# Performance work log

Hardware: AMD Instinct MI355X
Metric: run time of the kernel (lower is better)

The kernel has to match this reference:

```python
import jax, jax.numpy as jnp
import numpy as np

B, VH, VL, EP = 4, 130, 120, 256
DIN, DEP, D, H, NL = 256, 128, 512, 16, 8
HID = 4 * D

def _pe(x, base=1000.0):
    # sinusoidal positional encoding (base=1000 as in the module)
    L, Dm = x.shape[-2], x.shape[-1]
    pos = jnp.arange(L, dtype=jnp.float32)
    ch = jnp.arange(Dm, dtype=jnp.float32)
    ang = pos[:, None] / (base ** (2.0 * ch / ch[-1]))[None]
    enc = jnp.where(ch % 2 == 0, jnp.sin(ang), jnp.cos(ang))
    return x + enc

def _ln(x, g, b):
    m = x.mean(-1, keepdims=True)
    v = ((x - m) ** 2).mean(-1, keepdims=True)
    return (x - m) / jnp.sqrt(v + 1e-5) * g + b

def _gmha(x, rots, trans, mask_bias, qkv_w, out_w, out_b, g, b, r_s, d_s):
    # ESM3 geometric multi-head attention (algorithm 6)
    xn = _ln(x, g, b)
    qkv = (xn @ qkv_w.T).reshape(x.shape[0], x.shape[1], 5, H, 3)  # [B,L,5,H,3]
    qkv = jnp.einsum('brid,brfhd->brfhi', rots, qkv)               # rotate into global frame
    Qr, Kr, Qd, Kd, V = (qkv[..., f, :, :] for f in range(5))
    scale = 3.0 ** -0.5
    Ar = jnp.einsum('bihd,bjhd->bijh', Qr, Kr) * jax.nn.softplus(r_s) * scale
    qd = Qd + trans[:, :, None, :]
    kd = Kd + trans[:, :, None, :]
    dist = jnp.linalg.norm(qd[:, :, None] - kd[:, None], axis=-1)  # [B,i,j,H]
    logits = Ar - dist * jax.nn.softplus(d_s) * scale + mask_bias[..., None]
    A = jax.nn.softmax(logits, axis=2)
    o = jnp.einsum('bijh,bjhd->bihd', A, V)
    o = jnp.einsum('brji,brhj->brhi', rots, o)                     # rotate back (R^T)
    return o.reshape(x.shape[0], x.shape[1], H * 3) @ out_w.T + out_b

def _swiglu(x, g, b, w12, w3):
    # SwiGLU transition (dropout is identity in eval)
    h = _ln(x, g, b) @ w12.T
    a, v = jnp.split(h, 2, axis=-1)
    return (jax.nn.silu(a) * v) @ w3.T

def _forward(vh_x, vl_x, vh_rots, vh_trans, vl_rots, vl_trans, ep_feats, ep_rots, ep_trans,
             vh_emb_w, vl_emb_w, tgt_emb_w, qkv_w, out_w, out_b, ln_g, ln_b, r_scale, d_scale,
             ln2_g, ln2_b, w12, w3, out_vh_w, out_vh_gate_w, out_vh_gate_b,
             out_vl_w, out_vl_gate_w, out_vl_gate_b, vh_mask, vl_mask, ep_mask):
    emb = jnp.concatenate([_pe(vh_x @ vh_emb_w.T), _pe(vl_x @ vl_emb_w.T), ep_feats @ tgt_emb_w.T], axis=1)
    rots = jnp.concatenate([vh_rots, vl_rots, ep_rots], axis=1)
    trans = jnp.concatenate([vh_trans, vl_trans, ep_trans], axis=1)
    mask = jnp.concatenate([vh_mask, vl_mask, ep_mask], axis=1)
    mask_bias = jnp.where(mask[:, :, None] | mask[:, None, :], -1e9, 0.0)
    for i in range(NL):
        emb = emb + _gmha(emb, rots, trans, mask_bias, qkv_w[i], out_w[i], out_b[i],
                          ln_g[i], ln_b[i], r_scale[i], d_scale[i])
        emb = emb + _swiglu(emb, ln2_g[i], ln2_b[i], w12[i], w3[i])
    vh_e, vl_e = emb[:, :VH], emb[:, VH:VH + VL]
    vh_upd = (vh_e @ out_vh_w.T) * jax.nn.sigmoid(vh_e @ out_vh_gate_w.T + out_vh_gate_b)
    vl_upd = (vl_e @ out_vl_w.T) * jax.nn.sigmoid(vl_e @ out_vl_gate_w.T + out_vl_gate_b)
    vh_out = jnp.where(~vh_mask[..., None], vh_x + vh_upd, vh_x)
    vl_out = jnp.where(~vl_mask[..., None], vl_x + vl_upd, vl_x)
    return vh_out, vl_out

def setup_inputs():
    key = jax.random.key(0)
    ks = iter(jax.random.split(key, 40))
    s = 0.02
    return dict(
        vh_x=jax.random.normal(next(ks), (B, VH, DIN)),
        vl_x=jax.random.normal(next(ks), (B, VL, DIN)),
        vh_rots=jax.random.normal(next(ks), (B, VH, 3, 3)),
        vh_trans=jax.random.normal(next(ks), (B, VH, 3)),
        vl_rots=jax.random.normal(next(ks), (B, VL, 3, 3)),
        vl_trans=jax.random.normal(next(ks), (B, VL, 3)),
        ep_feats=jax.random.normal(next(ks), (B, EP, DEP)),
        ep_rots=jax.random.normal(next(ks), (B, EP, 3, 3)),
        ep_trans=jax.random.normal(next(ks), (B, EP, 3)),
        vh_mask=jnp.zeros((B, VH), dtype=bool),
        vl_mask=jnp.zeros((B, VL), dtype=bool),
        ep_mask=jax.random.randint(next(ks), (B, EP), 0, 2).astype(bool),
        vh_emb_w=jax.random.normal(next(ks), (D, DIN)) * s,
        vl_emb_w=jax.random.normal(next(ks), (D, DIN)) * s,
        tgt_emb_w=jax.random.normal(next(ks), (D, DEP)) * s,
        qkv_w=jax.random.normal(next(ks), (NL, H * 15, D)) * s,
        out_w=jax.random.normal(next(ks), (NL, D, H * 3)) * s,
        out_b=jnp.zeros((NL, D)),
        ln_g=jnp.ones((NL, D)), ln_b=jnp.zeros((NL, D)),
        r_scale=jnp.zeros((NL, H)), d_scale=jnp.zeros((NL, H)),
        ln2_g=jnp.ones((NL, D)), ln2_b=jnp.zeros((NL, D)),
        w12=jax.random.normal(next(ks), (NL, 2 * HID, D)) * s,
        w3=jax.random.normal(next(ks), (NL, D, HID)) * s,
        out_vh_w=jax.random.normal(next(ks), (DIN, D)) * s,
        out_vh_gate_w=jax.random.normal(next(ks), (DIN, D)) * s,
        out_vh_gate_b=jnp.full((DIN,), -2.0),
        out_vl_w=jax.random.normal(next(ks), (DIN, D)) * s,
        out_vl_gate_w=jax.random.normal(next(ks), (DIN, D)) * s,
        out_vl_gate_b=jnp.full((DIN,), -2.0),
    )

def reference(vh_x, vl_x, vh_rots, vh_trans, vl_rots, vl_trans, ep_feats, ep_rots, ep_trans,
              vh_mask, vl_mask, ep_mask,
              vh_emb_w, vl_emb_w, tgt_emb_w, qkv_w, out_w, out_b, ln_g, ln_b, r_scale, d_scale,
              ln2_g, ln2_b, w12, w3, out_vh_w, out_vh_gate_w, out_vh_gate_b,
              out_vl_w, out_vl_gate_w, out_vl_gate_b):
    return _forward(vh_x, vl_x, vh_rots, vh_trans, vl_rots, vl_trans, ep_feats, ep_rots, ep_trans,
                    vh_emb_w, vl_emb_w, tgt_emb_w, qkv_w, out_w, out_b, ln_g, ln_b, r_scale, d_scale,
                    ln2_g, ln2_b, w12, w3, out_vh_w, out_vh_gate_w, out_vh_gate_b,
                    out_vl_w, out_vl_gate_w, out_vl_gate_b, vh_mask, vl_mask, ep_mask)
```

## Files before the change

kernel.cpp:

```cpp
#include <hip/hip_runtime.h>
#include <hip/hip_bf16.h>
#include <math.h>
#include <stdint.h>

#define B_ 4
#define VH_ 130
#define VL_ 120
#define EP_ 256
#define R_ 506
#define RP_ 512
#define DIN_ 256
#define DEP_ 128
#define D_ 512
#define H_ 16
#define NL_ 8
#define HID_ 2048

#define MODE_STORE 0
#define MODE_ADD_BIAS 1

typedef _Float16 half8 __attribute__((ext_vector_type(8)));
typedef float f32x4 __attribute__((ext_vector_type(4)));

#define ASYNC16(ldsdst, gsrc)                                                  \
  __builtin_amdgcn_global_load_lds(                                            \
      (const __attribute__((address_space(1))) unsigned int*)(gsrc),           \
      (__attribute__((address_space(3))) unsigned int*)(ldsdst), 16, 0, 0)

__global__ __launch_bounds__(256) void gemm16sw_kernel(
    const _Float16* __restrict__ A, const _Float16* __restrict__ Wa,
    const _Float16* __restrict__ Wv, _Float16* __restrict__ Gh,
    int M, int K) {
  __shared__ _Float16 Al[4][4096];
  __shared__ _Float16 Ba[4][2048];
  __shared__ _Float16 Bv[4][2048];

  const int t = threadIdx.x;
  const int nbm = (M + 127) >> 7;
  const int nwg = gridDim.x;
  int bid = blockIdx.x;
  if ((nwg & 7) == 0) {
    int q = nwg >> 3;
    bid = (bid & 7) * q + (bid >> 3);
  }
  const int bm = bid % nbm, bn = bid / nbm;
  const int lane = t & 63;
  const int w = t >> 6;
  const int wm = w >> 1, wn = w & 1;

  const int r0 = t >> 2;
  const int cp = t & 3;
  const int gc = cp ^ ((r0 >> 1) & 3);
  int gr0 = bm * 128 + r0;       if (gr0 >= M) gr0 = M - 1;
  int gr1 = bm * 128 + 64 + r0;  if (gr1 >= M) gr1 = M - 1;
  const int gcol = bn * 64 + r0;
  const _Float16* pA0 = A + (size_t)gr0 * K + gc * 8;
  const _Float16* pA1 = A + (size_t)gr1 * K + gc * 8;
  const _Float16* pBa = Wa + (size_t)gcol * K + gc * 8;
  const _Float16* pBv = Wv + (size_t)gcol * K + gc * 8;

#define STAGE(buf, kt)                                                         \
  do {                                                                         \
    ASYNC16(&Al[buf][t * 8], pA0 + (size_t)(kt) * 32);                         \
    ASYNC16(&Al[buf][2048 + t * 8], pA1 + (size_t)(kt) * 32);                  \
    ASYNC16(&Ba[buf][t * 8], pBa + (size_t)(kt) * 32);                         \
    ASYNC16(&Bv[buf][t * 8], pBv + (size_t)(kt) * 32);                         \
  } while (0)

  f32x4 aca[4][2], acv[4][2];
#pragma unroll
  for (int i = 0; i < 4; i++)
#pragma unroll
    for (int j = 0; j < 2; j++) {
      aca[i][j] = (f32x4){0.f, 0.f, 0.f, 0.f};
      acv[i][j] = (f32x4){0.f, 0.f, 0.f, 0.f};
    }

  const int nt = K >> 5;
  STAGE(0, 0); STAGE(1, 1); STAGE(2, 2);

  const int rl = lane & 15;
  const int ca = (lane >> 4) ^ ((rl >> 1) & 3);
  for (int kt = 0; kt < nt; ++kt) {
    if (kt < nt - 2)       asm volatile("s_waitcnt vmcnt(8)" ::: "memory");
    else if (kt == nt - 2) asm volatile("s_waitcnt vmcnt(4)" ::: "memory");
    else                   asm volatile("s_waitcnt vmcnt(0)" ::: "memory");
    __builtin_amdgcn_s_barrier();
    const int buf = kt & 3;
    const _Float16* Ab  = &Al[buf][(wm * 64 + rl) * 32 + ca * 8];
    const _Float16* Bab = &Ba[buf][(wn * 32 + rl) * 32 + ca * 8];
    const _Float16* Bvb = &Bv[buf][(wn * 32 + rl) * 32 + ca * 8];
    half8 af[4], bfa[2], bfv[2];
#pragma unroll
    for (int i = 0; i < 4; i++) af[i] = *(const half8*)(Ab + i * 512);
#pragma unroll
    for (int j = 0; j < 2; j++) {
      bfa[j] = *(const half8*)(Bab + j * 512);
      bfv[j] = *(const half8*)(Bvb + j * 512);
    }
#pragma unroll
    for (int i = 0; i < 4; i++)
#pragma unroll
      for (int j = 0; j < 2; j++) {
        aca[i][j] = __builtin_amdgcn_mfma_f32_16x16x32_f16(af[i], bfa[j],
                                                           aca[i][j], 0, 0, 0);
        acv[i][j] = __builtin_amdgcn_mfma_f32_16x16x32_f16(af[i], bfv[j],
                                                           acv[i][j], 0, 0, 0);
      }
    if (kt + 3 < nt) STAGE((kt + 3) & 3, kt + 3);
  }
#undef STAGE

  const int rb = bm * 128 + wm * 64 + ((lane >> 4) << 2);
  const int cb = bn * 64 + wn * 32 + (lane & 15);
#pragma unroll
  for (int i = 0; i < 4; i++) {
#pragma unroll
    for (int j = 0; j < 2; j++) {
      int col = cb + j * 16;
#pragma unroll
      for (int q = 0; q < 4; q++) {
        int row = rb + i * 16 + q;
        if (row >= M) continue;
        float a = aca[i][j][q];
        float v = acv[i][j][q];
        Gh[(size_t)row * HID_ + col] = (_Float16)((a / (1.f + expf(-a))) * v);
      }
    }
  }
}

__global__ __launch_bounds__(256) void gemm16b_kernel(
    const _Float16* __restrict__ A, const _Float16* __restrict__ W,
    float* __restrict__ C, const float* __restrict__ bias,
    int M, int N, int K, int mode, int crpb, int cR, int cbase, int pe) {
  __shared__ _Float16 Al[4][2048];
  __shared__ _Float16 Bl[4][2048];

  const int t = threadIdx.x;
  const int nbm = (M + 63) >> 6;
  const int nwg = gridDim.x;
  int bid = blockIdx.x;
  if ((nwg & 7) == 0) {
    int q = nwg >> 3;
    bid = (bid & 7) * q + (bid >> 3);
  }
  const int bm = bid % nbm, bn = bid / nbm;
  const int lane = t & 63;
  const int w = t >> 6;
  const int wm = w >> 1, wn = w & 1;

  const int r0 = t >> 2;
  const int cp = t & 3;
  const int gc = cp ^ ((r0 >> 1) & 3);
  int gr = bm * 64 + r0;    if (gr >= M) gr = M - 1;
  int gcol = bn * 64 + r0;  if (gcol >= N) gcol = N - 1;
  const _Float16* pA = A + (size_t)gr * K + gc * 8;
  const _Float16* pB = W + (size_t)gcol * K + gc * 8;

#define STAGE(buf, kt)                                                         \
  do {                                                                         \
    ASYNC16(&Al[buf][t * 8], pA + (size_t)(kt) * 32);                          \
    ASYNC16(&Bl[buf][t * 8], pB + (size_t)(kt) * 32);                          \
  } while (0)

  f32x4 acc[2][2];
#pragma unroll
  for (int i = 0; i < 2; i++)
#pragma unroll
    for (int j = 0; j < 2; j++) acc[i][j] = (f32x4){0.f, 0.f, 0.f, 0.f};

  const int nt = K >> 5;
  STAGE(0, 0); STAGE(1, 1); STAGE(2, 2);

  const int rl = lane & 15;
  const int ca = (lane >> 4) ^ ((rl >> 1) & 3);
  for (int kt = 0; kt < nt; ++kt) {
    if (kt < nt - 2)       asm volatile("s_waitcnt vmcnt(4)" ::: "memory");
    else if (kt == nt - 2) asm volatile("s_waitcnt vmcnt(2)" ::: "memory");
    else                   asm volatile("s_waitcnt vmcnt(0)" ::: "memory");
    __builtin_amdgcn_s_barrier();
    const int buf = kt & 3;
    half8 af[2], bf[2];
#pragma unroll
    for (int i = 0; i < 2; i++)
      af[i] = *(const half8*)&Al[buf][(wm * 32 + i * 16 + rl) * 32 + ca * 8];
#pragma unroll
    for (int j = 0; j < 2; j++)
      bf[j] = *(const half8*)&Bl[buf][(wn * 32 + j * 16 + rl) * 32 + ca * 8];
#pragma unroll
    for (int i = 0; i < 2; i++)
#pragma unroll
      for (int j = 0; j < 2; j++)
        acc[i][j] = __builtin_amdgcn_mfma_f32_16x16x32_f16(af[i], bf[j],
                                                           acc[i][j], 0, 0, 0);
    if (kt + 3 < nt) STAGE((kt + 3) & 3, kt + 3);
  }
#undef STAGE

  const float PEK = -0.02703623196464017f;
  const int rb = bm * 64 + wm * 32 + ((lane >> 4) << 2);
  const int cb = bn * 64 + wn * 32 + (lane & 15);
#pragma unroll
  for (int i = 0; i < 2; i++) {
#pragma unroll
    for (int j = 0; j < 2; j++) {
      int col = cb + j * 16;
      if (col >= N) continue;
#pragma unroll
      for (int q = 0; q < 4; q++) {
        int row = rb + i * 16 + q;
        if (row >= M) continue;
        int crow = (row / crpb) * cR + cbase + row % crpb;
        size_t idx = (size_t)crow * N + col;
        float v = acc[i][j][q];
        if (pe) {
          float pos = (float)(row % crpb);
          float ang = pos * expf((float)col * PEK);
          v += (col & 1) ? cosf(ang) : sinf(ang);
        }
        if (mode == MODE_STORE) C[idx] = v;
        else {
          float bb = bias ? bias[col] : 0.f;
          C[idx] = C[idx] + v + bb;
        }
      }
    }
  }
}

__global__ __launch_bounds__(256) void gemm16gate_kernel(
    const _Float16* __restrict__ A, const _Float16* __restrict__ Wv,
    const _Float16* __restrict__ Wg, const float* __restrict__ x,
    const float* __restrict__ gb, const int* __restrict__ mask,
    float* __restrict__ out, int M, int K, int arpb, int aR, int abase) {
  __shared__ _Float16 Al[4][2048];
  __shared__ _Float16 Bva[4][2048];
  __shared__ _Float16 Bga[4][2048];

  const int t = threadIdx.x;
  const int nbm = (M + 63) >> 6;
  const int nwg = gridDim.x;
  int bid = blockIdx.x;
  if ((nwg & 7) == 0) {
    int q = nwg >> 3;
    bid = (bid & 7) * q + (bid >> 3);
  }
  const int bm = bid % nbm, bn = bid / nbm;
  const int lane = t & 63;
  const int w = t >> 6;
  const int wm = w >> 1, wn = w & 1;

  const int r0 = t >> 2;
  const int cp = t & 3;
  const int gc = cp ^ ((r0 >> 1) & 3);
  int gr = bm * 64 + r0;  if (gr >= M) gr = M - 1;
  int ar = (gr / arpb) * aR + abase + gr % arpb;
  const int gcol = bn * 64 + r0;
  const _Float16* pA  = A + (size_t)ar * K + gc * 8;
  const _Float16* pBv = Wv + (size_t)gcol * K + gc * 8;
  const _Float16* pBg = Wg + (size_t)gcol * K + gc * 8;

#define STAGE(buf, kt)                                                         \
  do {                                                                         \
    ASYNC16(&Al[buf][t * 8], pA + (size_t)(kt) * 32);                          \
    ASYNC16(&Bva[buf][t * 8], pBv + (size_t)(kt) * 32);                        \
    ASYNC16(&Bga[buf][t * 8], pBg + (size_t)(kt) * 32);                        \
  } while (0)

  f32x4 acv[2][2], acg[2][2];
#pragma unroll
  for (int i = 0; i < 2; i++)
#pragma unroll
    for (int j = 0; j < 2; j++) {
      acv[i][j] = (f32x4){0.f, 0.f, 0.f, 0.f};
      acg[i][j] = (f32x4){0.f, 0.f, 0.f, 0.f};
    }

  const int nt = K >> 5;
  STAGE(0, 0); STAGE(1, 1); STAGE(2, 2);

  const int rl = lane & 15;
  const int ca = (lane >> 4) ^ ((rl >> 1) & 3);
  for (int kt = 0; kt < nt; ++kt) {
    if (kt < nt - 2)       asm volatile("s_waitcnt vmcnt(6)" ::: "memory");
    else if (kt == nt - 2) asm volatile("s_waitcnt vmcnt(3)" ::: "memory");
    else                   asm volatile("s_waitcnt vmcnt(0)" ::: "memory");
    __builtin_amdgcn_s_barrier();
    const int buf = kt & 3;
    half8 af[2], bv[2], bg2[2];
#pragma unroll
    for (int i = 0; i < 2; i++)
      af[i] = *(const half8*)&Al[buf][(wm * 32 + i * 16 + rl) * 32 + ca * 8];
#pragma unroll
    for (int j = 0; j < 2; j++) {
      bv[j] = *(const half8*)&Bva[buf][(wn * 32 + j * 16 + rl) * 32 + ca * 8];
      bg2[j] = *(const half8*)&Bga[buf][(wn * 32 + j * 16 + rl) * 32 + ca * 8];
    }
#pragma unroll
    for (int i = 0; i < 2; i++)
#pragma unroll
      for (int j = 0; j < 2; j++) {
        acv[i][j] = __builtin_amdgcn_mfma_f32_16x16x32_f16(af[i], bv[j],
                                                           acv[i][j], 0, 0, 0);
        acg[i][j] = __builtin_amdgcn_mfma_f32_16x16x32_f16(af[i], bg2[j],
                                                           acg[i][j], 0, 0, 0);
      }
    if (kt + 3 < nt) STAGE((kt + 3) & 3, kt + 3);
  }
#undef STAGE

  const int rb = bm * 64 + wm * 32 + ((lane >> 4) << 2);
  const int cb = bn * 64 + wn * 32 + (lane & 15);
#pragma unroll
  for (int i = 0; i < 2; i++) {
#pragma unroll
    for (int j = 0; j < 2; j++) {
      int col = cb + j * 16;
#pragma unroll
      for (int q = 0; q < 4; q++) {
        int row = rb + i * 16 + q;
        if (row >= M) continue;
        size_t idx = (size_t)row * DIN_ + col;
        float xv = x[idx];
        float res;
        if (mask[row]) {
          res = xv;
        } else {
          float gate = 1.f / (1.f + expf(-(acg[i][j][q] + gb[col])));
          res = xv + acv[i][j][q] * gate;
        }
        out[idx] = res;
      }
    }
  }
}

__global__ __launch_bounds__(256) void ln_kernel(
    const float* __restrict__ x, const float* __restrict__ g,
    const float* __restrict__ b, _Float16* __restrict__ out) {
  const int row = blockIdx.x;
  const int t = threadIdx.x;
  const float* xr = x + (size_t)row * D_;
  float v0 = xr[t], v1 = xr[t + 256];
  float s = v0 + v1, s2 = v0 * v0 + v1 * v1;
#pragma unroll
  for (int o = 32; o > 0; o >>= 1) {
    s += __shfl_down(s, o);
    s2 += __shfl_down(s2, o);
  }
  __shared__ float w1[4], w2[4], mv[2];
  const int w = t >> 6;
  if ((t & 63) == 0) { w1[w] = s; w2[w] = s2; }
  __syncthreads();
  if (t == 0) {
    float ss = w1[0] + w1[1] + w1[2] + w1[3];
    float ss2 = w2[0] + w2[1] + w2[2] + w2[3];
    float mean = ss * (1.f / D_);
    float var = ss2 * (1.f / D_) - mean * mean;
    mv[0] = mean;
    mv[1] = rsqrtf(var + 1e-5f);
  }
  __syncthreads();
  float mean = mv[0], inv = mv[1];
  _Float16* orow = out + (size_t)row * D_;
  orow[t] = (_Float16)((v0 - mean) * inv * g[t] + b[t]);
  orow[t + 256] = (_Float16)((v1 - mean) * inv * g[t + 256] + b[t + 256]);
}

struct ThSegs {
  const float* src[13];
  _Float16* dst[13];
  int cum[14];
};
__global__ void tohalf_multi_kernel(ThSegs sg) {
  int total = sg.cum[13];
  for (int i = blockIdx.x * blockDim.x + threadIdx.x; i < total;
       i += gridDim.x * blockDim.x) {
    int s = 0;
    while (i >= sg.cum[s + 1]) s++;
    int off = i - sg.cum[s];
    const float4* p = (const float4*)(sg.src[s] + (size_t)off * 8);
    float4 x = p[0], y = p[1];
    half8 h = {(_Float16)x.x, (_Float16)x.y, (_Float16)x.z, (_Float16)x.w,
               (_Float16)y.x, (_Float16)y.y, (_Float16)y.z, (_Float16)y.w};
    *(half8*)(sg.dst[s] + (size_t)off * 8) = h;
  }
}

__global__ void tohalf_kernel(const float* __restrict__ src,
                              _Float16* __restrict__ dst, int n8) {
  for (int i = blockIdx.x * blockDim.x + threadIdx.x; i < n8;
       i += gridDim.x * blockDim.x) {
    const float4* s = (const float4*)(src + (size_t)i * 8);
    float4 x = s[0], y = s[1];
    half8 h = {(_Float16)x.x, (_Float16)x.y, (_Float16)x.z, (_Float16)x.w,
               (_Float16)y.x, (_Float16)y.y, (_Float16)y.z, (_Float16)y.w};
    *(half8*)(dst + (size_t)i * 8) = h;
  }
}

__global__ void transpose_ow_kernel(const float* __restrict__ out_w,
                                    float* __restrict__ owT) {
  int idx = blockIdx.x * blockDim.x + threadIdx.x;
  const int total = NL_ * 48 * D_;
  if (idx >= total) return;
  int l = idx / (48 * D_);
  int rem = idx % (48 * D_);
  int k = rem / D_;
  int c = rem % D_;
  owT[idx] = out_w[(size_t)l * D_ * 48 + (size_t)c * 48 + k];
}

__global__ void prep_kernel(
    const float* __restrict__ vh_rots, const float* __restrict__ vh_trans,
    const float* __restrict__ vl_rots, const float* __restrict__ vl_trans,
    const float* __restrict__ ep_rots, const float* __restrict__ ep_trans,
    const int* __restrict__ vh_mask, const int* __restrict__ vl_mask,
    const int* __restrict__ ep_mask, float* __restrict__ rots,
    float* __restrict__ trans, int* __restrict__ mask,
    int* __restrict__ maskp, float* __restrict__ Kt, float* __restrict__ PKt,
    float* __restrict__ Vt) {
  int idx = blockIdx.x * blockDim.x + threadIdx.x;
  if (idx < B_ * RP_) {
    int b = idx >> 9, r = idx & (RP_ - 1);
    if (r >= R_) {
      maskp[idx] = 1;
      return;
    }
    const float* sr; const float* st; int sm;
    if (r < VH_) {
      sr = vh_rots + (size_t)(b * VH_ + r) * 9;
      st = vh_trans + (size_t)(b * VH_ + r) * 3;
      sm = vh_mask[b * VH_ + r];
    } else if (r < VH_ + VL_) {
      int rr = r - VH_;
      sr = vl_rots + (size_t)(b * VL_ + rr) * 9;
      st = vl_trans + (size_t)(b * VL_ + rr) * 3;
      sm = vl_mask[b * VL_ + rr];
    } else {
      int rr = r - VH_ - VL_;
      sr = ep_rots + (size_t)(b * EP_ + rr) * 9;
      st = ep_trans + (size_t)(b * EP_ + rr) * 3;
      sm = ep_mask[b * EP_ + rr];
    }
    int lin = b * R_ + r;
    maskp[idx] = sm;
    mask[lin] = sm;
#pragma unroll
    for (int k = 0; k < 9; k++) rots[(size_t)lin * 9 + k] = sr[k];
#pragma unroll
    for (int k = 0; k < 3; k++) trans[(size_t)lin * 3 + k] = st[k];
  } else {
    int p = idx - B_ * RP_;
    const int per = B_ * H_ * 3 * (RP_ - R_);
    if (p >= 3 * per) return;
    int a = p / per;
    int q = p % per;
    int chan = q / (RP_ - R_), jj = q % (RP_ - R_);
    float* dst = (a == 0) ? Kt : (a == 1) ? PKt : Vt;
    dst[(size_t)chan * RP_ + R_ + jj] = 0.f;
  }
}

__global__ __launch_bounds__(128) void rotate_kernel(
    const float* __restrict__ qkv_raw, const float* __restrict__ rots,
    const float* __restrict__ trans, float* __restrict__ Qrow,
    float* __restrict__ PQrow, float* __restrict__ Kt,
    float* __restrict__ PKt, float* __restrict__ Vt) {
  const int blk = blockIdx.x;
  const int b = blk / R_;
  const int r = blk % R_;
  const int t = threadIdx.x;
  __shared__ float Rm[9], tr[3], raw[240];
  if (t < 9) Rm[t] = rots[(size_t)blk * 9 + t];
  if (t >= 9 && t < 12) tr[t - 9] = trans[(size_t)blk * 3 + (t - 9)];
  for (int i = t; i < 240; i += 128) raw[i] = qkv_raw[(size_t)blk * 240 + i];
  __syncthreads();
  if (t < 80) {
    int f = t / 16, h = t % 16;
    float x = raw[f * 48 + h * 3 + 0];
    float y = raw[f * 48 + h * 3 + 1];
    float z = raw[f * 48 + h * 3 + 2];
    float r0 = Rm[0] * x + Rm[1] * y + Rm[2] * z;
    float r1 = Rm[3] * x + Rm[4] * y + Rm[5] * z;
    float r2 = Rm[6] * x + Rm[7] * y + Rm[8] * z;
    if (f == 2 || f == 3) { r0 += tr[0]; r1 += tr[1]; r2 += tr[2]; }
    if (f == 0 || f == 2) {
      float* dst = (f == 0) ? Qrow : PQrow;
      size_t o = (size_t)blk * 48 + h * 3;
      dst[o] = r0; dst[o + 1] = r1; dst[o + 2] = r2;
    } else {
      float* dst = (f == 1) ? Kt : (f == 3) ? PKt : Vt;
      size_t base = ((size_t)(b * H_ + h) * 3) * RP_ + r;
      dst[base] = r0; dst[base + RP_] = r1; dst[base + 2 * RP_] = r2;
    }
  }
}

__global__ __launch_bounds__(256) void attn2_kernel(
    const float* __restrict__ Qrow, const float* __restrict__ PQrow,
    const float* __restrict__ Kt, const float* __restrict__ PKt,
    const float* __restrict__ Vt, const float* __restrict__ rots,
    const int* __restrict__ mask, const int* __restrict__ maskp,
    const float* __restrict__ rs, const float* __restrict__ ds,
    const float* __restrict__ owT, const float* __restrict__ out_b,
    float* __restrict__ emb) {
  const int blk = blockIdx.x;
  const int b = blk / (R_ / 2);
  const int ip = blk % (R_ / 2);
  const int i0 = ip * 2;
  const int t = threadIdx.x;
  const int lane = t & 63;
  const int w = t >> 6;

  __shared__ float qs[2][48], ps[2][48], og[2][48];
  __shared__ float crs[16], cds[16];
  __shared__ int mi[2];

  if (t < 96) {
    int io = t / 48, k2 = t % 48;
    int i = i0 + io;
    qs[io][k2] = Qrow[((size_t)(b * R_ + i)) * 48 + k2];
    ps[io][k2] = PQrow[((size_t)(b * R_ + i)) * 48 + k2];
  } else if (t < 112) {
    int h = t - 96;
    const float sc = 0.57735026918962576f;
    crs[h] = log1pf(expf(rs[h])) * sc;
    cds[h] = log1pf(expf(ds[h])) * sc;
  } else if (t < 114) {
    mi[t - 112] = mask[b * R_ + i0 + (t - 112)];
  }
  __syncthreads();

  float mb[8];
#pragma unroll
  for (int jb = 0; jb < 8; jb++) {
    int j = jb * 64 + lane;
    mb[jb] = maskp[b * RP_ + j] ? -1e9f : 0.f;
  }
  const float bi0 = mi[0] ? -1e9f : 0.f;
  const float bi1 = mi[1] ? -1e9f : 0.f;

  for (int hh = 0; hh < 4; hh++) {
    const int h = hh * 4 + w;
    const float sA = crs[h], sD = cds[h];
    const float qx0 = qs[0][h * 3], qy0 = qs[0][h * 3 + 1], qz0 = qs[0][h * 3 + 2];
    const float px0 = ps[0][h * 3], py0 = ps[0][h * 3 + 1], pz0 = ps[0][h * 3 + 2];
    const float qx1 = qs[1][h * 3], qy1 = qs[1][h * 3 + 1], qz1 = qs[1][h * 3 + 2];
    const float px1 = ps[1][h * 3], py1 = ps[1][h * 3 + 1], pz1 = ps[1][h * 3 + 2];
    const float* kb = Kt + ((size_t)(b * H_ + h) * 3) * RP_;
    const float* pb = PKt + ((size_t)(b * H_ + h) * 3) * RP_;
    const float* vb = Vt + ((size_t)(b * H_ + h) * 3) * RP_;

    float l0[8], l1[8];
    float m0 = -3e38f, m1 = -3e38f;
#pragma unroll
    for (int jb = 0; jb < 8; jb++) {
      int j = jb * 64 + lane;
      float kx = kb[j], ky = kb[j + RP_], kz = kb[j + 2 * RP_];
      float pkx = pb[j], pky = pb[j + RP_], pkz = pb[j + 2 * RP_];
      float dx0 = px0 - pkx, dy0 = py0 - pky, dz0 = pz0 - pkz;
      float d0 = sqrtf(dx0 * dx0 + dy0 * dy0 + dz0 * dz0);
      l0[jb] = (qx0 * kx + qy0 * ky + qz0 * kz) * sA - d0 * sD + mb[jb] + bi0;
      m0 = fmaxf(m0, l0[jb]);
      float dx1 = px1 - pkx, dy1 = py1 - pky, dz1 = pz1 - pkz;
      float d1 = sqrtf(dx1 * dx1 + dy1 * dy1 + dz1 * dz1);
      l1[jb] = (qx1 * kx + qy1 * ky + qz1 * kz) * sA - d1 * sD + mb[jb] + bi1;
      m1 = fmaxf(m1, l1[jb]);
    }
#pragma unroll
    for (int s = 1; s < 64; s <<= 1) {
      m0 = fmaxf(m0, __shfl_xor(m0, s));
      m1 = fmaxf(m1, __shfl_xor(m1, s));
    }
    float s0 = 0.f, s1 = 0.f;
    float ox0 = 0.f, oy0 = 0.f, oz0 = 0.f, ox1 = 0.f, oy1 = 0.f, oz1 = 0.f;
#pragma unroll
    for (int jb = 0; jb < 8; jb++) {
      int j = jb * 64 + lane;
      float p0 = expf(l0[jb] - m0);
      float p1 = expf(l1[jb] - m1);
      s0 += p0; s1 += p1;
      float vx = vb[j], vy = vb[j + RP_], vz = vb[j + 2 * RP_];
      ox0 += p0 * vx; oy0 += p0 * vy; oz0 += p0 * vz;
      ox1 += p1 * vx; oy1 += p1 * vy; oz1 += p1 * vz;
    }
#pragma unroll
    for (int s = 1; s < 64; s <<= 1) {
      s0 += __shfl_xor(s0, s); s1 += __shfl_xor(s1, s);
      ox0 += __shfl_xor(ox0, s); oy0 += __shfl_xor(oy0, s); oz0 += __shfl_xor(oz0, s);
      ox1 += __shfl_xor(ox1, s); oy1 += __shfl_xor(oy1, s); oz1 += __shfl_xor(oz1, s);
    }
    if (lane == 0) {
      og[0][h * 3] = ox0 / s0; og[0][h * 3 + 1] = oy0 / s0; og[0][h * 3 + 2] = oz0 / s0;
      og[1][h * 3] = ox1 / s1; og[1][h * 3 + 1] = oy1 / s1; og[1][h * 3 + 2] = oz1 / s1;
    }
  }
  __syncthreads();
  float r0v0 = 0.f, r0v1 = 0.f;
  if (t < 48) {
    int h = t / 3, i3 = t % 3;
    const float* Rm0 = rots + ((size_t)(b * R_ + i0)) * 9;
    const float* Rm1 = rots + ((size_t)(b * R_ + i0 + 1)) * 9;
    r0v0 = Rm0[0 + i3] * og[0][h * 3 + 0] + Rm0[3 + i3] * og[0][h * 3 + 1] +
           Rm0[6 + i3] * og[0][h * 3 + 2];
    r0v1 = Rm1[0 + i3] * og[1][h * 3 + 0] + Rm1[3 + i3] * og[1][h * 3 + 1] +
           Rm1[6 + i3] * og[1][h * 3 + 2];
  }
  __syncthreads();
  if (t < 48) { og[0][t] = r0v0; og[1][t] = r0v1; }
  __syncthreads();
#pragma unroll
  for (int io = 0; io < 2; io++) {
    float* erow = emb + ((size_t)(b * R_ + i0 + io)) * D_;
#pragma unroll
    for (int half = 0; half < 2; half++) {
      int c = half * 256 + t;
      float a0 = 0.f, a1 = 0.f, a2 = 0.f, a3 = 0.f;
#pragma unroll
      for (int k = 0; k < 48; k += 4) {
        a0 += og[io][k + 0] * owT[(size_t)(k + 0) * D_ + c];
        a1 += og[io][k + 1] * owT[(size_t)(k + 1) * D_ + c];
        a2 += og[io][k + 2] * owT[(size_t)(k + 2) * D_ + c];
        a3 += og[io][k + 3] * owT[(size_t)(k + 3) * D_ + c];
      }
      erow[c] += out_b[c] + ((a0 + a1) + (a2 + a3));
    }
  }
}

extern "C" void kernel_launch(void* const* d_in, const int* in_sizes, int n_in,
                              void* d_out, int out_size, void* d_ws, size_t ws_size,
                              hipStream_t stream) {
  const float* vh_x = (const float*)d_in[0];
  const float* vl_x = (const float*)d_in[1];
  const float* vh_rots = (const float*)d_in[2];
  const float* vh_trans = (const float*)d_in[3];
  const float* vl_rots = (const float*)d_in[4];
  const float* vl_trans = (const float*)d_in[5];
  const float* ep_feats = (const float*)d_in[6];
  const float* ep_rots = (const float*)d_in[7];
  const float* ep_trans = (const float*)d_in[8];
  const int* vh_mask = (const int*)d_in[9];
  const int* vl_mask = (const int*)d_in[10];
  const int* ep_mask = (const int*)d_in[11];
  const float* vh_emb_w = (const float*)d_in[12];
  const float* vl_emb_w = (const float*)d_in[13];
  const float* tgt_emb_w = (const float*)d_in[14];
  const float* qkv_w = (const float*)d_in[15];
  const float* out_w = (const float*)d_in[16];
  const float* out_b = (const float*)d_in[17];
  const float* ln_g = (const float*)d_in[18];
  const float* ln_b = (const float*)d_in[19];
  const float* r_scale = (const float*)d_in[20];
  const float* d_scale = (const float*)d_in[21];
  const float* ln2_g = (const float*)d_in[22];
  const float* ln2_b = (const float*)d_in[23];
  const float* w12 = (const float*)d_in[24];
  const float* w3 = (const float*)d_in[25];
  const float* out_vh_w = (const float*)d_in[26];
  const float* out_vh_gate_w = (const float*)d_in[27];
  const float* out_vh_gate_b = (const float*)d_in[28];
  const float* out_vl_w = (const float*)d_in[29];
  const float* out_vl_gate_w = (const float*)d_in[30];
  const float* out_vl_gate_b = (const float*)d_in[31];

  const int BR = B_ * R_;

  uint8_t* P = (uint8_t*)d_ws;
  auto alloc = [&](size_t bytes) {
    uint8_t* p = P;
    P += (bytes + 255) & ~(size_t)255;
    return p;
  };
  float* emb = (float*)alloc((size_t)BR * D_ * 4);
  _Float16* xnh = (_Float16*)alloc((size_t)BR * D_ * 2);
  float* qkvr = (float*)alloc((size_t)BR * 240 * 4);
  float* Qrow = (float*)alloc((size_t)BR * 48 * 4);
  float* PQrow = (float*)alloc((size_t)BR * 48 * 4);
  float* Kt = (float*)alloc((size_t)B_ * H_ * 3 * RP_ * 4);
  float* PKt = (float*)alloc((size_t)B_ * H_ * 3 * RP_ * 4);
  float* Vt = (float*)alloc((size_t)B_ * H_ * 3 * RP_ * 4);
  _Float16* ghalf = (_Float16*)alloc((size_t)BR * HID_ * 2);
  float* rots_c = (float*)alloc((size_t)BR * 9 * 4);
  float* trans_c = (float*)alloc((size_t)BR * 3 * 4);
  int* mask_c = (int*)alloc((size_t)BR * 4);
  int* maskp = (int*)alloc((size_t)B_ * RP_ * 4);
  float* owT = (float*)alloc((size_t)NL_ * 48 * D_ * 4);
  _Float16* embh = (_Float16*)alloc((size_t)BR * D_ * 2);
  _Float16* qkvh = (_Float16*)alloc((size_t)NL_ * 240 * D_ * 2);
  _Float16* w12h = (_Float16*)alloc((size_t)NL_ * 2 * HID_ * D_ * 2);
  _Float16* w3h = (_Float16*)alloc((size_t)NL_ * D_ * HID_ * 2);
  _Float16* vhxh = (_Float16*)alloc((size_t)B_ * VH_ * DIN_ * 2);
  _Float16* vlxh = (_Float16*)alloc((size_t)B_ * VL_ * DIN_ * 2);
  _Float16* eph = (_Float16*)alloc((size_t)B_ * EP_ * DEP_ * 2);
  _Float16* vhewh = (_Float16*)alloc((size_t)D_ * DIN_ * 2);
  _Float16* vlewh = (_Float16*)alloc((size_t)D_ * DIN_ * 2);
  _Float16* tgewh = (_Float16*)alloc((size_t)D_ * DEP_ * 2);
  _Float16* ovhw = (_Float16*)alloc((size_t)DIN_ * D_ * 2);
  _Float16* ovhgw = (_Float16*)alloc((size_t)DIN_ * D_ * 2);
  _Float16* ovlw = (_Float16*)alloc((size_t)DIN_ * D_ * 2);
  _Float16* ovlgw = (_Float16*)alloc((size_t)DIN_ * D_ * 2);

  {
    ThSegs sg;
    const float* srcs[13] = {qkv_w, w12, w3, vh_x, vl_x, ep_feats,
                             vh_emb_w, vl_emb_w, tgt_emb_w,
                             out_vh_w, out_vh_gate_w, out_vl_w, out_vl_gate_w};
    _Float16* dsts[13] = {qkvh, w12h, w3h, vhxh, vlxh, eph,
                          vhewh, vlewh, tgewh, ovhw, ovhgw, ovlw, ovlgw};
    int n8s[13] = {NL_ * 240 * D_ / 8, NL_ * 2 * HID_ * D_ / 8,
                   NL_ * D_ * HID_ / 8, B_ * VH_ * DIN_ / 8,
                   B_ * VL_ * DIN_ / 8, B_ * EP_ * DEP_ / 8,
                   D_ * DIN_ / 8, D_ * DIN_ / 8, D_ * DEP_ / 8,
                   DIN_ * D_ / 8, DIN_ * D_ / 8, DIN_ * D_ / 8, DIN_ * D_ / 8};
    int c = 0;
    for (int i = 0; i < 13; i++) {
      sg.src[i] = srcs[i]; sg.dst[i] = dsts[i];
      sg.cum[i] = c; c += n8s[i];
    }
    sg.cum[13] = c;
    tohalf_multi_kernel<<<2048, 256, 0, stream>>>(sg);
  }

  {
    int total = NL_ * 48 * D_;
    transpose_ow_kernel<<<(total + 255) / 256, 256, 0, stream>>>(out_w, owT);
  }

  {
    int total = B_ * RP_ + 3 * B_ * H_ * 3 * (RP_ - R_);
    prep_kernel<<<(total + 255) / 256, 256, 0, stream>>>(
        vh_rots, vh_trans, vl_rots, vl_trans, ep_rots, ep_trans, vh_mask,
        vl_mask, ep_mask, rots_c, trans_c, mask_c, maskp, Kt, PKt, Vt);
  }

  auto gemm16b = [&](const _Float16* A, const _Float16* W, float* C,
                     const float* bias, int M, int N, int K, int mode,
                     int crpb, int cR, int cbase, int pe) {
    int nbm = (M + 63) / 64, nbn = (N + 63) / 64;
    gemm16b_kernel<<<nbm * nbn, 256, 0, stream>>>(A, W, C, bias, M, N, K, mode,
                                                  crpb, cR, cbase, pe);
  };

  gemm16b(vhxh, vhewh, emb, nullptr, B_ * VH_, D_, DIN_, MODE_STORE,
          VH_, R_, 0, 1);
  gemm16b(vlxh, vlewh, emb, nullptr, B_ * VL_, D_, DIN_, MODE_STORE,
          VL_, R_, VH_, 1);
  gemm16b(eph, tgewh, emb, nullptr, B_ * EP_, D_, DEP_, MODE_STORE,
          EP_, R_, VH_ + VL_, 0);

  for (int l = 0; l < NL_; l++) {
    const _Float16* qwh = qkvh + (size_t)l * 240 * D_;
    const float* owTl = owT + (size_t)l * 48 * D_;
    const float* obias = out_b + (size_t)l * D_;
    const float* lg = ln_g + (size_t)l * D_;
    const float* lb = ln_b + (size_t)l * D_;
    const float* l2g = ln2_g + (size_t)l * D_;
    const float* l2b = ln2_b + (size_t)l * D_;
    const float* rs = r_scale + (size_t)l * H_;
    const float* dsc = d_scale + (size_t)l * H_;
    const _Float16* w12ah = w12h + (size_t)l * 2 * HID_ * D_;
    const _Float16* w12bh = w12ah + (size_t)HID_ * D_;
    const _Float16* w3lh = w3h + (size_t)l * D_ * HID_;

    ln_kernel<<<BR, 256, 0, stream>>>(emb, lg, lb, xnh);
    gemm16b(xnh, qwh, qkvr, nullptr, BR, 240, D_, MODE_STORE, BR, BR, 0, 0);
    rotate_kernel<<<BR, 128, 0, stream>>>(qkvr, rots_c, trans_c, Qrow, PQrow,
                                          Kt, PKt, Vt);
    attn2_kernel<<<B_ * (R_ / 2), 256, 0, stream>>>(
        Qrow, PQrow, Kt, PKt, Vt, rots_c, mask_c, maskp, rs, dsc, owTl, obias,
        emb);

    ln_kernel<<<BR, 256, 0, stream>>>(emb, l2g, l2b, xnh);
    {
      int nbm = (BR + 127) / 128, nbn = HID_ / 64;
      gemm16sw_kernel<<<nbm * nbn, 256, 0, stream>>>(xnh, w12ah, w12bh, ghalf,
                                                     BR, D_);
    }
    gemm16b(ghalf, w3lh, emb, nullptr, BR, D_, HID_, MODE_ADD_BIAS,
            BR, BR, 0, 0);
  }

  tohalf_kernel<<<1024, 256, 0, stream>>>(emb, embh, BR * D_ / 8);
  {
    int M = B_ * VH_;
    int nbm = (M + 63) / 64;
    gemm16gate_kernel<<<nbm * 4, 256, 0, stream>>>(
        embh, ovhw, ovhgw, vh_x, out_vh_gate_b, vh_mask, (float*)d_out, M, D_,
        VH_, R_, 0);
  }
  {
    int M = B_ * VL_;
    int nbm = (M + 63) / 64;
    gemm16gate_kernel<<<nbm * 4, 256, 0, stream>>>(
        embh, ovlw, ovlgw, vl_x, out_vl_gate_b, vl_mask,
        (float*)d_out + (size_t)B_ * VH_ * DIN_, M, D_, VL_, R_, VH_);
  }
}
```

Before: 1.108 ms.

## Use one wave per head in attention and convert sixteen floats per thread

The attention kernel now launches 1024 threads per block, so each of the 16 heads gets its own wavefront instead of four waves looping over four heads each. The output projection is spread across all 1024 threads, one output element per thread. Separately, the fp32-to-fp16 conversion kernel now handles 16 elements per thread instead of 8, which halves the per-element segment-search overhead. The larger blocks raise per-block parallelism but cap register use under a 1024-thread launch bound and may reduce how many blocks fit per CU.

```diff
diff --git a/kernel.cpp b/kernel.cpp
--- a/kernel.cpp
+++ b/kernel.cpp
@@ -380,11 +380,15 @@
     int s = 0;
     while (i >= sg.cum[s + 1]) s++;
     int off = i - sg.cum[s];
-    const float4* p = (const float4*)(sg.src[s] + (size_t)off * 8);
-    float4 x = p[0], y = p[1];
-    half8 h = {(_Float16)x.x, (_Float16)x.y, (_Float16)x.z, (_Float16)x.w,
-               (_Float16)y.x, (_Float16)y.y, (_Float16)y.z, (_Float16)y.w};
-    *(half8*)(sg.dst[s] + (size_t)off * 8) = h;
+    const float4* p = (const float4*)(sg.src[s] + (size_t)off * 16);
+    float4 x = p[0], y = p[1], z = p[2], w = p[3];
+    half8 h0 = {(_Float16)x.x, (_Float16)x.y, (_Float16)x.z, (_Float16)x.w,
+                (_Float16)y.x, (_Float16)y.y, (_Float16)y.z, (_Float16)y.w};
+    half8 h1 = {(_Float16)z.x, (_Float16)z.y, (_Float16)z.z, (_Float16)z.w,
+                (_Float16)w.x, (_Float16)w.y, (_Float16)w.z, (_Float16)w.w};
+    half8* d = (half8*)(sg.dst[s] + (size_t)off * 16);
+    d[0] = h0;
+    d[1] = h1;
   }
 }
 
@@ -498,7 +502,7 @@
   }
 }
 
-__global__ __launch_bounds__(256) void attn2_kernel(
+__global__ __launch_bounds__(1024) void attn2_kernel(
     const float* __restrict__ Qrow, const float* __restrict__ PQrow,
     const float* __restrict__ Kt, const float* __restrict__ PKt,
     const float* __restrict__ Vt, const float* __restrict__ rots,
@@ -512,7 +516,7 @@
   const int i0 = ip * 2;
   const int t = threadIdx.x;
   const int lane = t & 63;
-  const int w = t >> 6;
+  const int h = t >> 6;
 
   __shared__ float qs[2][48], ps[2][48], og[2][48];
   __shared__ float crs[16], cds[16];
@@ -524,10 +528,10 @@
     qs[io][k2] = Qrow[((size_t)(b * R_ + i)) * 48 + k2];
     ps[io][k2] = PQrow[((size_t)(b * R_ + i)) * 48 + k2];
   } else if (t < 112) {
-    int h = t - 96;
+    int hh = t - 96;
     const float sc = 0.57735026918962576f;
-    crs[h] = log1pf(expf(rs[h])) * sc;
-    cds[h] = log1pf(expf(ds[h])) * sc;
+    crs[hh] = log1pf(expf(rs[hh])) * sc;
+    cds[hh] = log1pf(expf(ds[hh])) * sc;
   } else if (t < 114) {
     mi[t - 112] = mask[b * R_ + i0 + (t - 112)];
   }
@@ -542,8 +546,7 @@
   const float bi0 = mi[0] ? -1e9f : 0.f;
   const float bi1 = mi[1] ? -1e9f : 0.f;
 
-  for (int hh = 0; hh < 4; hh++) {
-    const int h = hh * 4 + w;
+  {
     const float sA = crs[h], sD = cds[h];
     const float qx0 = qs[0][h * 3], qy0 = qs[0][h * 3 + 1], qz0 = qs[0][h * 3 + 2];
     const float px0 = ps[0][h * 3], py0 = ps[0][h * 3 + 1], pz0 = ps[0][h * 3 + 2];
@@ -600,33 +603,30 @@
   __syncthreads();
   float r0v0 = 0.f, r0v1 = 0.f;
   if (t < 48) {
-    int h = t / 3, i3 = t % 3;
+    int hh = t / 3, i3 = t % 3;
     const float* Rm0 = rots + ((size_t)(b * R_ + i0)) * 9;
     const float* Rm1 = rots + ((size_t)(b * R_ + i0 + 1)) * 9;
-    r0v0 = Rm0[0 + i3] * og[0][h * 3 + 0] + Rm0[3 + i3] * og[0][h * 3 + 1] +
-           Rm0[6 + i3] * og[0][h * 3 + 2];
-    r0v1 = Rm1[0 + i3] * og[1][h * 3 + 0] + Rm1[3 + i3] * og[1][h * 3 + 1] +
-           Rm1[6 + i3] * og[1][h * 3 + 2];
+    r0v0 = Rm0[0 + i3] * og[0][hh * 3 + 0] + Rm0[3 + i3] * og[0][hh * 3 + 1] +
+           Rm0[6 + i3] * og[0][hh * 3 + 2];
+    r0v1 = Rm1[0 + i3] * og[1][hh * 3 + 0] + Rm1[3 + i3] * og[1][hh * 3 + 1] +
+           Rm1[6 + i3] * og[1][hh * 3 + 2];
   }
   __syncthreads();
   if (t < 48) { og[0][t] = r0v0; og[1][t] = r0v1; }
   __syncthreads();
-#pragma unroll
-  for (int io = 0; io < 2; io++) {
+  {
+    const int io = t >> 9;
+    const int c = t & 511;
     float* erow = emb + ((size_t)(b * R_ + i0 + io)) * D_;
-#pragma unroll
-    for (int half = 0; half < 2; half++) {
-      int c = half * 256 + t;
-      float a0 = 0.f, a1 = 0.f, a2 = 0.f, a3 = 0.f;
-#pragma unroll
-      for (int k = 0; k < 48; k += 4) {
-        a0 += og[io][k + 0] * owT[(size_t)(k + 0) * D_ + c];
-        a1 += og[io][k + 1] * owT[(size_t)(k + 1) * D_ + c];
-        a2 += og[io][k + 2] * owT[(size_t)(k + 2) * D_ + c];
-        a3 += og[io][k + 3] * owT[(size_t)(k + 3) * D_ + c];
-      }
-      erow[c] += out_b[c] + ((a0 + a1) + (a2 + a3));
-    }
+    float a0 = 0.f, a1 = 0.f, a2 = 0.f, a3 = 0.f;
+#pragma unroll
+    for (int k = 0; k < 48; k += 4) {
+      a0 += og[io][k + 0] * owT[(size_t)(k + 0) * D_ + c];
+      a1 += og[io][k + 1] * owT[(size_t)(k + 1) * D_ + c];
+      a2 += og[io][k + 2] * owT[(size_t)(k + 2) * D_ + c];
+      a3 += og[io][k + 3] * owT[(size_t)(k + 3) * D_ + c];
+    }
+    erow[c] += out_b[c] + ((a0 + a1) + (a2 + a3));
   }
 }
 
@@ -710,15 +710,16 @@
                              out_vh_w, out_vh_gate_w, out_vl_w, out_vl_gate_w};
     _Float16* dsts[13] = {qkvh, w12h, w3h, vhxh, vlxh, eph,
                           vhewh, vlewh, tgewh, ovhw, ovhgw, ovlw, ovlgw};
-    int n8s[13] = {NL_ * 240 * D_ / 8, NL_ * 2 * HID_ * D_ / 8,
-                   NL_ * D_ * HID_ / 8, B_ * VH_ * DIN_ / 8,
-                   B_ * VL_ * DIN_ / 8, B_ * EP_ * DEP_ / 8,
-                   D_ * DIN_ / 8, D_ * DIN_ / 8, D_ * DEP_ / 8,
-                   DIN_ * D_ / 8, DIN_ * D_ / 8, DIN_ * D_ / 8, DIN_ * D_ / 8};
+    int n16s[13] = {NL_ * 240 * D_ / 16, NL_ * 2 * HID_ * D_ / 16,
+                    NL_ * D_ * HID_ / 16, B_ * VH_ * DIN_ / 16,
+                    B_ * VL_ * DIN_ / 16, B_ * EP_ * DEP_ / 16,
+                    D_ * DIN_ / 16, D_ * DIN_ / 16, D_ * DEP_ / 16,
+                    DIN_ * D_ / 16, DIN_ * D_ / 16, DIN_ * D_ / 16,
+                    DIN_ * D_ / 16};
     int c = 0;
     for (int i = 0; i < 13; i++) {
       sg.src[i] = srcs[i]; sg.dst[i] = dsts[i];
-      sg.cum[i] = c; c += n8s[i];
+      sg.cum[i] = c; c += n16s[i];
     }
     sg.cum[13] = c;
     tohalf_multi_kernel<<<2048, 256, 0, stream>>>(sg);
@@ -769,7 +770,7 @@
     gemm16b(xnh, qwh, qkvr, nullptr, BR, 240, D_, MODE_STORE, BR, BR, 0, 0);
     rotate_kernel<<<BR, 128, 0, stream>>>(qkvr, rots_c, trans_c, Qrow, PQrow,
                                           Kt, PKt, Vt);
-    attn2_kernel<<<B_ * (R_ / 2), 256, 0, stream>>>(
+    attn2_kernel<<<B_ * (R_ / 2), 1024, 0, stream>>>(
         Qrow, PQrow, Kt, PKt, Vt, rots_c, mask_c, maskp, rs, dsc, owTl, obias,
         emb);
 
```

Result: slower. 1.200 ms (+8.3%).
